# Kernel optimization log

Measured on AMD Instinct MI355X. Metric: run time of the kernel, lower is better.

## Reference

```python
import jax, jax.numpy as jnp
import numpy as np

N, E, HID, ED, L, H, D = 65536, 262144, 256, 64, 2, 8, 32
FF = 4 * HID
A_START = 8192  # first action gripper node; nodes [A_START:] are the T*K action nodes


def _ln(x, s, b, eps=1e-5):
    mu = jnp.mean(x, -1, keepdims=True)
    var = jnp.var(x, -1, keepdims=True)
    return (x - mu) * jax.lax.rsqrt(var + eps) * s + b


def _gnn_forward(x, edge_attr, edge_index, Wq, Wk, Wv, WeK, WeV, Wo,
                 ln1_s, ln1_b, ffn_w1, ffn_b1, ffn_w2, ffn_b2, ln2_s, ln2_b):
    # Hetero graph transformer over the single ('gripper','action','gripper') relation:
    # per-layer edge-indexed gather -> multi-head attention with edge features ->
    # segment softmax over incoming edges -> scatter-aggregate -> residual/LN/FFN.
    n = x.shape[0]
    e = edge_attr.shape[0]
    src, dst = edge_index[0], edge_index[1]
    inv_sqrt_d = np.float32(1.0 / np.sqrt(D))
    for l in range(Wq.shape[0]):
        q = (x @ Wq[l]).reshape(n, H, D)
        k = (x @ Wk[l]).reshape(n, H, D)
        v = (x @ Wv[l]).reshape(n, H, D)
        kj = k[src] + (edge_attr @ WeK[l]).reshape(e, H, D)  # [E,H,D] gathered keys + edge bias
        vj = v[src] + (edge_attr @ WeV[l]).reshape(e, H, D)
        score = jnp.einsum('ehd,ehd->eh', q[dst], kj) * inv_sqrt_d  # [E,H]
        smax = jax.ops.segment_max(score, dst, num_segments=n)
        p = jnp.exp(score - smax[dst])
        denom = jax.ops.segment_sum(p, dst, num_segments=n)
        alpha = p / denom[dst]  # segment softmax over incoming edges
        agg = jax.ops.segment_sum((alpha[..., None] * vj).reshape(e, H * D), dst, num_segments=n)
        x = _ln(x + agg @ Wo[l], ln1_s[l], ln1_b[l])
        hid = jax.nn.gelu(x @ ffn_w1[l] + ffn_b1[l], approximate=False) @ ffn_w2[l] + ffn_b2[l]
        x = _ln(x + hid, ln2_s[l], ln2_b[l])
    return x


def setup_inputs() -> dict:
    key = jax.random.key(0)
    ks = iter(jax.random.split(key, 16))
    w = lambda shape: jax.random.normal(next(ks), shape, jnp.float32) * 0.05
    return {
        "all_gripper_feats": jax.random.normal(next(ks), (N, HID), jnp.float32),
        "edge_attr": jax.random.normal(next(ks), (E, ED), jnp.float32),
        "Wq": w((L, HID, H * D)), "Wk": w((L, HID, H * D)), "Wv": w((L, HID, H * D)),
        "WeK": w((L, ED, H * D)), "WeV": w((L, ED, H * D)), "Wo": w((L, H * D, HID)),
        "ln1_s": jnp.ones((L, HID), jnp.float32), "ln1_b": jnp.zeros((L, HID), jnp.float32),
        "ffn_w1": w((L, HID, FF)), "ffn_b1": jnp.zeros((L, FF), jnp.float32),
        "ffn_w2": w((L, FF, HID)), "ffn_b2": jnp.zeros((L, HID), jnp.float32),
        "ln2_s": jnp.ones((L, HID), jnp.float32), "ln2_b": jnp.zeros((L, HID), jnp.float32),
        "head_w1": w((HID, HID)), "head_b1": jnp.zeros((HID,), jnp.float32),
        "head_w2": w((HID, 7)), "head_b2": jnp.zeros((7,), jnp.float32),
        "edge_index": jax.random.randint(next(ks), (2, E), 0, N),
        "action_start": A_START,
    }


def reference(all_gripper_feats, edge_attr, Wq, Wk, Wv, WeK, WeV, Wo,
              ln1_s, ln1_b, ffn_w1, ffn_b1, ffn_w2, ffn_b2, ln2_s, ln2_b,
              head_w1, head_b1, head_w2, head_b2, edge_index, action_start):
    x = _gnn_forward(all_gripper_feats, edge_attr, edge_index, Wq, Wk, Wv, WeK, WeV, Wo,
                     ln1_s, ln1_b, ffn_w1, ffn_b1, ffn_w2, ffn_b2, ln2_s, ln2_b)
    a = x[action_start:]  # action gripper nodes (T*K, hidden)
    return jax.nn.gelu(a @ head_w1 + head_b1, approximate=False) @ head_w2 + head_b2  # (T*K, 7)
```

## Files before the change

kernel.cpp:

```cpp
#include <hip/hip_runtime.h>
#include <hip/hip_bf16.h>
#include <math.h>

#define NN     65536
#define NE     262144
#define HIDN   256
#define EDIM   64
#define NHEAD  8
#define FFN    1024
#define ASTART 8192
#define NACT   (NN - ASTART)
#define NCH    32768
#define NCHP   (NCH + 128)
#define NCHUNK (NE / NCH)
#define DPC    (NN / NCHUNK)
#define RCH    32768

typedef __attribute__((ext_vector_type(8))) short short8;
typedef __attribute__((ext_vector_type(4))) short short4v;
typedef __attribute__((ext_vector_type(4))) float float4v;
typedef __hip_bfloat16 bf16;

__device__ __forceinline__ float b2f(short s) {
    union { unsigned u; float f; } c;
    c.u = ((unsigned)(unsigned short)s) << 16;
    return c.f;
}
__device__ __forceinline__ short f2b(float f) {
    __hip_bfloat16 h = __float2bfloat16(f);
    return *reinterpret_cast<short*>(&h);
}
__device__ __forceinline__ float gelu_fast(float v) {
    const float x  = v * 0.70710678118654752f;
    const float ax = fabsf(x);
    const float t  = __builtin_amdgcn_rcpf(1.0f + 0.3275911f * ax);
    const float y  = t * (0.254829592f + t * (-0.284496736f + t * (1.421413741f +
                     t * (-1.453152027f + t * 1.061405429f))));
    const float e  = __expf(-x * x);
    float erf = 1.0f - y * e;
    erf = copysignf(erf, x);
    return 0.5f * v * (1.0f + erf);
}
__device__ __forceinline__ void gload16(const void* g, void* l) {
    __builtin_amdgcn_global_load_lds(
        (const __attribute__((address_space(1))) void*)(uintptr_t)g,
        (__attribute__((address_space(3))) void*)(unsigned)(uintptr_t)l,
        16, 0, 0);
}

__global__ void convert_kernel(const float* __restrict__ src,
                               bf16* __restrict__ dst, int n) {
    int i = blockIdx.x * 256 + threadIdx.x;
    if (i < n) dst[i] = __float2bfloat16(src[i]);
}
__global__ void convert4_kernel(const float* __restrict__ src,
                                bf16* __restrict__ dst, int n4) {
    int i = blockIdx.x * 256 + threadIdx.x;
    if (i >= n4) return;
    float4v f = *(const float4v*)(src + (size_t)i * 4);
    short4v o;
    #pragma unroll
    for (int j = 0; j < 4; ++j) o[j] = f2b(f[j]);
    *(short4v*)((short*)dst + (size_t)i * 4) = o;
}

__global__ void transpose_kernel(const float* __restrict__ src,
                                 bf16* __restrict__ dst, int R, int Cc) {
    int idx = blockIdx.x * 256 + threadIdx.x;
    if (idx >= R * Cc) return;
    int r = idx / Cc, c = idx - r * Cc;
    dst[(size_t)c * R + r] = __float2bfloat16(src[idx]);
}

__global__ void hist_kernel(const int* __restrict__ dstI, int* __restrict__ cnt) {
    int i = blockIdx.x * 256 + threadIdx.x;
    if (i < NE) atomicAdd(&cnt[dstI[i]], 1);
}
__global__ void scan1_kernel(const int* __restrict__ cnt, int* __restrict__ rp,
                             int* __restrict__ bsum) {
    __shared__ int s[256];
    int t = threadIdx.x, i = blockIdx.x * 256 + t;
    int v = cnt[i]; s[t] = v; __syncthreads();
    for (int off = 1; off < 256; off <<= 1) {
        int x = (t >= off) ? s[t - off] : 0; __syncthreads();
        s[t] += x; __syncthreads();
    }
    rp[i] = s[t] - v;
    if (t == 255) bsum[blockIdx.x] = s[255];
}
__global__ void scan2_kernel(int* __restrict__ bsum) {
    __shared__ int s[256];
    int t = threadIdx.x; int v = bsum[t]; s[t] = v; __syncthreads();
    for (int off = 1; off < 256; off <<= 1) {
        int x = (t >= off) ? s[t - off] : 0; __syncthreads();
        s[t] += x; __syncthreads();
    }
    bsum[t] = s[t] - v;
}
__global__ void scan3_kernel(int* __restrict__ rp, const int* __restrict__ bsum,
                             int* __restrict__ cursor) {
    int i = blockIdx.x * 256 + threadIdx.x;
    int v = rp[i] + bsum[i >> 8];
    rp[i] = v; cursor[i] = v;
    if (i == 0) rp[NN] = NE;
}
__global__ void scatter_kernel(const int* __restrict__ srcI, const int* __restrict__ dstI,
                               int* __restrict__ cursor, int* __restrict__ perm,
                               int* __restrict__ src_s, int* __restrict__ dst_s) {
    int e = blockIdx.x * 256 + threadIdx.x;
    if (e >= NE) return;
    int d = dstI[e];
    int pos = atomicAdd(&cursor[d], 1);
    perm[pos] = e; src_s[pos] = srcI[e]; dst_s[pos] = d;
}

template<int AMODE, bool DO_GELU>
__global__ __launch_bounds__(256) void gemm_kernel(
    const void* __restrict__ A,
    const bf16* __restrict__ BT,
    const bf16* __restrict__ bias,
    bf16* __restrict__ C,
    int M, int Nn, int K,
    const int* __restrict__ perm, int permN)
{
    __shared__ __align__(16) short Ls[4][128 * 32];

    const int gx   = gridDim.x;
    const int nwg  = gx * gridDim.y;
    const int orig = blockIdx.y * gx + blockIdx.x;
    const int q8   = nwg >> 3, r8 = nwg & 7;
    const int xcd  = orig & 7, rk = orig >> 3;
    const int nid  = (xcd < r8 ? xcd * (q8 + 1) : r8 * (q8 + 1) + (xcd - r8) * q8) + rk;
    const int by   = nid / gx;
    const int bx   = nid - by * gx;

    const int t    = threadIdx.x;
    const int wave = t >> 6;
    const int lane = t & 63;
    const int l15  = lane & 15;
    const int quad = lane >> 4;
    const int wm   = (wave & 1) * 64;
    const int wn   = (wave >> 1) * 64;
    const int bm   = by * 128;
    const int bn   = bx * 128;
    const int srow = t >> 2;
    const int sw   = srow & 3;
    const int scolB = ((t & 3) ^ sw) * 8;
    const int scolA = (t & 3) * 8;

    const short* Ab = (const short*)A  + (size_t)(bm + srow) * K + scolB;
    const short* Bb = (const short*)BT + (size_t)(bn + srow) * K + scolB;
    const float* Af0 = nullptr;
    const float* Af1 = nullptr;
    if (AMODE == 1) {
        Af0 = (const float*)A + (size_t)(bm + srow) * K + scolA;
        Af1 = Af0 + (size_t)64 * K;
    } else if (AMODE == 2) {
        int i0 = bm + srow;       if (i0 >= permN) i0 = permN - 1;
        int i1 = bm + 64 + srow;  if (i1 >= permN) i1 = permN - 1;
        const int pr0 = perm[i0];
        const int pr1 = perm[i1];
        Af0 = (const float*)A + (size_t)pr0 * K + scolA;
        Af1 = (const float*)A + (size_t)pr1 * K + scolA;
    }
    const int offW  = wave * 1024;
    const int offTs = (t * 16) ^ (sw << 4);
    const int qs16  = (quad ^ (l15 & 3)) * 16;

    float4v acc[4][4];
    #pragma unroll
    for (int i = 0; i < 4; ++i)
        #pragma unroll
        for (int j = 0; j < 4; ++j) acc[i][j] = (float4v){0.f, 0.f, 0.f, 0.f};

    const int nt = K >> 5;

    auto STAGE = [&](int b, int k0) {
        char* lA = (char*)Ls[b];
        char* lB = (char*)Ls[2 + b];
        if (AMODE == 0) {
            gload16(Ab + k0,                  lA + offW);
            gload16(Ab + (size_t)64 * K + k0, lA + 4096 + offW);
        } else {
            #pragma unroll
            for (int i = 0; i < 2; ++i) {
                const float* s = (i ? Af1 : Af0) + k0;
                float4v f0 = *(const float4v*)s;
                float4v f1 = *(const float4v*)(s + 4);
                short8 w;
                #pragma unroll
                for (int j = 0; j < 4; ++j) { w[j] = f2b(f0[j]); w[4 + j] = f2b(f1[j]); }
                *(short8*)(lA + i * 4096 + offTs) = w;
            }
        }
        gload16(Bb + k0,                  lB + offW);
        gload16(Bb + (size_t)64 * K + k0, lB + 4096 + offW);
    };

    STAGE(0, 0);
    __syncthreads();

    for (int kt = 0; kt < nt; ++kt) {
        const int cur = kt & 1;
        if (kt + 1 < nt) STAGE(cur ^ 1, (kt + 1) * 32);

        const char* lA = (const char*)Ls[cur];
        const char* lB = (const char*)Ls[2 + cur];
        short8 afr[4], bfr[4];
        #pragma unroll
        for (int i = 0; i < 4; ++i)
            afr[i] = *(const short8*)(lA + (wm + i * 16 + l15) * 64 + qs16);
        #pragma unroll
        for (int j = 0; j < 4; ++j)
            bfr[j] = *(const short8*)(lB + (wn + j * 16 + l15) * 64 + qs16);
        #pragma unroll
        for (int i = 0; i < 4; ++i)
            #pragma unroll
            for (int j = 0; j < 4; ++j)
                acc[i][j] = __builtin_amdgcn_mfma_f32_16x16x32_bf16(afr[i], bfr[j], acc[i][j], 0, 0, 0);
        __syncthreads();
    }

    short* Ct = (short*)Ls;
    #pragma unroll
    for (int j = 0; j < 4; ++j) {
        const int col  = wn + j * 16 + l15;
        const int pc   = col ^ (quad << 4);
        const float bv = bias ? b2f(((const short*)bias)[bn + col]) : 0.0f;
        #pragma unroll
        for (int i = 0; i < 4; ++i) {
            const int row0 = wm + i * 16 + quad * 4;
            #pragma unroll
            for (int r = 0; r < 4; ++r) {
                float v = acc[i][j][r] + bv;
                if (DO_GELU) v = gelu_fast(v);
                Ct[(row0 + r) * 128 + pc] = f2b(v);
            }
        }
    }
    __syncthreads();
    #pragma unroll
    for (int it = 0; it < 8; ++it) {
        const int row = wave * 32 + it + ((lane >> 4) << 3);
        const int cs  = (lane & 15) * 8;
        const int pcs = cs ^ (((row >> 2) & 3) << 4);
        short8 w = *(const short8*)&Ct[row * 128 + pcs];
        *(short8*)((short*)C + (size_t)(bm + row) * Nn + bn + cs) = w;
    }
}

__global__ __launch_bounds__(256) void score_kernel(
    const bf16* __restrict__ q, const bf16* __restrict__ k,
    const bf16* __restrict__ eK,
    const int* __restrict__ src_s, const int* __restrict__ dst_s,
    short* __restrict__ pbuf, int e0, int qkstride)
{
    const int p = e0 + blockIdx.x * 4 + (threadIdx.x >> 6);
    const int lane = threadIdx.x & 63;
    const int s = src_s[p], d = dst_s[p];
    const int off = lane * 4;

    const short4v qv = *(const short4v*)((const short*)q  + (size_t)d * qkstride + off);
    const short4v kv = *(const short4v*)((const short*)k  + (size_t)s * qkstride + off);
    const short4v ev = *(const short4v*)((const short*)eK + (size_t)(p - e0) * HIDN + off);
    float x = 0.f;
    #pragma unroll
    for (int j = 0; j < 4; ++j) x += b2f(qv[j]) * (b2f(kv[j]) + b2f(ev[j]));
    x += __shfl_xor(x, 1);
    x += __shfl_xor(x, 2);
    x += __shfl_xor(x, 4);
    if ((lane & 7) == 0) {
        const float sc = fminf(fmaxf(x * 0.17677669529663689f, -30.f), 30.f);
        pbuf[(size_t)p * NHEAD + (lane >> 3)] = f2b(expf(sc));
    }
}

__global__ __launch_bounds__(256) void agg_kernel(
    const short* __restrict__ pbuf, const bf16* __restrict__ v,
    const bf16* __restrict__ eV,
    const int* __restrict__ src_s, const int* __restrict__ rp,
    float* __restrict__ agg, int e0, int e1x, int dlo)
{
    const int d = dlo + blockIdx.x * 4 + (threadIdx.x >> 6);
    const int lane = threadIdx.x & 63;
    const int es = rp[d], ee = rp[d + 1];
    if (es < e0 || es >= e1x) return;
    const int h = lane >> 3, off = lane * 4;

    float a0 = 0.f, a1 = 0.f, a2 = 0.f, a3 = 0.f;
    if (es < ee) {
        float den = 0.f;
        for (int p = es; p < ee; ++p) den += b2f(pbuf[(size_t)p * NHEAD + h]);
        const float rden = 1.0f / den;
        for (int p = es; p < ee; ++p) {
            const float al = b2f(pbuf[(size_t)p * NHEAD + h]) * rden;
            const int s = src_s[p];
            const short4v vv = *(const short4v*)((const short*)v  + (size_t)s * HIDN + off);
            const short4v ev = *(const short4v*)((const short*)eV + (size_t)(p - e0) * HIDN + off);
            a0 += al * (b2f(vv[0]) + b2f(ev[0]));
            a1 += al * (b2f(vv[1]) + b2f(ev[1]));
            a2 += al * (b2f(vv[2]) + b2f(ev[2]));
            a3 += al * (b2f(vv[3]) + b2f(ev[3]));
        }
    }
    *(float4v*)(agg + (size_t)d * HIDN + off) = (float4v){a0, a1, a2, a3};
}

__global__ __launch_bounds__(256) void ln_kernel(
    bf16* __restrict__ x, const bf16* __restrict__ t,
    const bf16* __restrict__ sc, const bf16* __restrict__ bi, int r0)
{
    const int row = r0 + blockIdx.x * 4 + (threadIdx.x >> 6);
    const int lane = threadIdx.x & 63;
    const size_t base = (size_t)row * HIDN + lane * 4;
    const size_t tbase = (size_t)(row - r0) * HIDN + lane * 4;
    const short4v xv = *(const short4v*)((const short*)x + base);
    const short4v tv = *(const short4v*)((const short*)t + tbase);
    float v[4];
    #pragma unroll
    for (int j = 0; j < 4; ++j) v[j] = b2f(xv[j]) + b2f(tv[j]);
    float sum = v[0] + v[1] + v[2] + v[3];
    float ssq = v[0]*v[0] + v[1]*v[1] + v[2]*v[2] + v[3]*v[3];
    #pragma unroll
    for (int m = 1; m < 64; m <<= 1) { sum += __shfl_xor(sum, m); ssq += __shfl_xor(ssq, m); }
    const float mean = sum * (1.0f / 256.0f);
    const float var  = fmaxf(ssq * (1.0f / 256.0f) - mean * mean, 0.0f);
    const float rstd = rsqrtf(var + 1e-5f);
    const short4v sv = *(const short4v*)((const short*)sc + lane * 4);
    const short4v bv = *(const short4v*)((const short*)bi + lane * 4);
    short4v out;
    #pragma unroll
    for (int j = 0; j < 4; ++j)
        out[j] = f2b((v[j] - mean) * rstd * b2f(sv[j]) + b2f(bv[j]));
    *(short4v*)((short*)x + base) = out;
}

__global__ __launch_bounds__(256) void head2_kernel(
    const bf16* __restrict__ h1, const bf16* __restrict__ w2T,
    const bf16* __restrict__ b2, float* __restrict__ out)
{
    const int row = blockIdx.x * 4 + (threadIdx.x >> 6);
    const int lane = threadIdx.x & 63;
    const int off = lane * 4;
    const short4v hv = *(const short4v*)((const short*)h1 + (size_t)row * HIDN + off);
    float hf[4];
    #pragma unroll
    for (int j = 0; j < 4; ++j) hf[j] = b2f(hv[j]);
    float acc[7];
    #pragma unroll
    for (int jc = 0; jc < 7; ++jc) {
        const short4v wv = *(const short4v*)((const short*)w2T + jc * HIDN + off);
        float a = hf[0]*b2f(wv[0]) + hf[1]*b2f(wv[1]) + hf[2]*b2f(wv[2]) + hf[3]*b2f(wv[3]);
        #pragma unroll
        for (int m = 1; m < 64; m <<= 1) a += __shfl_xor(a, m);
        acc[jc] = a;
    }
    if (lane < 7) {
        float r = lane == 0 ? acc[0] : lane == 1 ? acc[1] : lane == 2 ? acc[2] :
                  lane == 3 ? acc[3] : lane == 4 ? acc[4] : lane == 5 ? acc[5] : acc[6];
        out[(size_t)row * 7 + lane] = r + b2f(((const short*)b2)[lane]);
    }
}

extern "C" void kernel_launch(void* const* d_in, const int* in_sizes, int n_in,
                              void* d_out, int out_size, void* d_ws, size_t ws_size,
                              hipStream_t stream)
{
    const float* xin   = (const float*)d_in[0];
    const float* eattr = (const float*)d_in[1];
    const float* Wq    = (const float*)d_in[2];
    const float* Wk    = (const float*)d_in[3];
    const float* Wv    = (const float*)d_in[4];
    const float* WeK   = (const float*)d_in[5];
    const float* WeV   = (const float*)d_in[6];
    const float* Wo    = (const float*)d_in[7];
    const float* ln1s  = (const float*)d_in[8];
    const float* ln1b  = (const float*)d_in[9];
    const float* fw1   = (const float*)d_in[10];
    const float* fb1   = (const float*)d_in[11];
    const float* fw2   = (const float*)d_in[12];
    const float* fb2   = (const float*)d_in[13];
    const float* ln2s  = (const float*)d_in[14];
    const float* ln2b  = (const float*)d_in[15];
    const float* hw1   = (const float*)d_in[16];
    const float* hb1   = (const float*)d_in[17];
    const float* hw2   = (const float*)d_in[18];
    const float* hb2   = (const float*)d_in[19];
    const int*  eidx   = (const int*)d_in[20];
    const int*  srcI   = eidx;
    const int*  dstI   = eidx + NE;

    char* base = (char*)d_ws;
    size_t off = 0;
    auto carve = [&](size_t bytes) -> char* {
        char* p = base + off;
        off += (bytes + 255) & ~(size_t)255;
        return p;
    };
    bf16*  x_b    = (bf16*) carve((size_t)NN * HIDN * 2);
    bf16*  qk_b   = (bf16*) carve((size_t)NN * 2 * HIDN * 2);
    bf16*  v_b    = (bf16*) carve((size_t)NN * HIDN * 2);
    bf16*  echunk = (bf16*) carve((size_t)NCHP * HIDN * 2);
    short* pbuf   = (short*)carve((size_t)NE * NHEAD * 2);
    int*   perm   = (int*)  carve((size_t)NE * 4);
    int*   src_s  = (int*)  carve((size_t)NE * 4);
    int*   dst_s  = (int*)  carve((size_t)NE * 4);
    int*   rowp   = (int*)  carve((size_t)(NN + 1) * 4);
    bf16*  WqkT   = (bf16*) carve((size_t)2 * HIDN * HIDN * 2);
    bf16*  WvT    = (bf16*) carve((size_t)HIDN * HIDN * 2);
    bf16*  WoT    = (bf16*) carve((size_t)HIDN * HIDN * 2);
    bf16*  WeKT   = (bf16*) carve((size_t)HIDN * EDIM * 2);
    bf16*  WeVT   = (bf16*) carve((size_t)HIDN * EDIM * 2);
    bf16*  W1T    = (bf16*) carve((size_t)FFN * HIDN * 2);
    bf16*  W2T    = (bf16*) carve((size_t)HIDN * FFN * 2);
    bf16*  HW1T   = (bf16*) carve((size_t)HIDN * HIDN * 2);
    bf16*  HW2T   = (bf16*) carve((size_t)8 * HIDN * 2);
    bf16*  c_ln1s = (bf16*) carve((size_t)2 * HIDN * 2);
    bf16*  c_ln1b = (bf16*) carve((size_t)2 * HIDN * 2);
    bf16*  c_ln2s = (bf16*) carve((size_t)2 * HIDN * 2);
    bf16*  c_ln2b = (bf16*) carve((size_t)2 * HIDN * 2);
    bf16*  c_fb1  = (bf16*) carve((size_t)2 * FFN * 2);
    bf16*  c_fb2  = (bf16*) carve((size_t)2 * HIDN * 2);
    bf16*  c_hb1  = (bf16*) carve((size_t)HIDN * 2);
    bf16*  c_hb2  = (bf16*) carve((size_t)16 * 2);
    if (off > ws_size) return;

    int* cnt    = (int*)echunk;
    int* cursor = cnt + NN;
    int* bsum   = cursor + NN;
    float* agg    = (float*)qk_b;
    bf16*  tmp_b  = v_b;
    bf16*  hid    = qk_b;
    bf16*  ffnout = v_b;

    const int TB = 256;
    #define GRID1(n) dim3(((n) + TB - 1) / TB)

    convert4_kernel<<<GRID1(NN * HIDN / 4), TB, 0, stream>>>(xin, x_b, NN * HIDN / 4);
    convert_kernel<<<GRID1(2 * HIDN), TB, 0, stream>>>(ln1s, c_ln1s, 2 * HIDN);
    convert_kernel<<<GRID1(2 * HIDN), TB, 0, stream>>>(ln1b, c_ln1b, 2 * HIDN);
    convert_kernel<<<GRID1(2 * HIDN), TB, 0, stream>>>(ln2s, c_ln2s, 2 * HIDN);
    convert_kernel<<<GRID1(2 * HIDN), TB, 0, stream>>>(ln2b, c_ln2b, 2 * HIDN);
    convert_kernel<<<GRID1(2 * FFN), TB, 0, stream>>>(fb1, c_fb1, 2 * FFN);
    convert_kernel<<<GRID1(2 * HIDN), TB, 0, stream>>>(fb2, c_fb2, 2 * HIDN);
    convert_kernel<<<GRID1(HIDN), TB, 0, stream>>>(hb1, c_hb1, HIDN);
    convert_kernel<<<1, TB, 0, stream>>>(hb2, c_hb2, 7);
    transpose_kernel<<<GRID1(HIDN * HIDN), TB, 0, stream>>>(hw1, HW1T, HIDN, HIDN);
    transpose_kernel<<<GRID1(HIDN * 7), TB, 0, stream>>>(hw2, HW2T, HIDN, 7);

    hipMemsetAsync(cnt, 0, (size_t)NN * 4, stream);
    hist_kernel<<<GRID1(NE), TB, 0, stream>>>(dstI, cnt);
    scan1_kernel<<<NN / 256, 256, 0, stream>>>(cnt, rowp, bsum);
    scan2_kernel<<<1, 256, 0, stream>>>(bsum);
    scan3_kernel<<<NN / 256, 256, 0, stream>>>(rowp, bsum, cursor);
    scatter_kernel<<<GRID1(NE), TB, 0, stream>>>(srcI, dstI, cursor, perm, src_s, dst_s);

    for (int l = 0; l < 2; ++l) {
        transpose_kernel<<<GRID1(HIDN * HIDN), TB, 0, stream>>>(Wq + (size_t)l*HIDN*HIDN, WqkT, HIDN, HIDN);
        transpose_kernel<<<GRID1(HIDN * HIDN), TB, 0, stream>>>(Wk + (size_t)l*HIDN*HIDN, WqkT + (size_t)HIDN*HIDN, HIDN, HIDN);
        transpose_kernel<<<GRID1(HIDN * HIDN), TB, 0, stream>>>(Wv + (size_t)l*HIDN*HIDN, WvT, HIDN, HIDN);
        transpose_kernel<<<GRID1(EDIM * HIDN), TB, 0, stream>>>(WeK + (size_t)l*EDIM*HIDN, WeKT, EDIM, HIDN);
        transpose_kernel<<<GRID1(EDIM * HIDN), TB, 0, stream>>>(WeV + (size_t)l*EDIM*HIDN, WeVT, EDIM, HIDN);
        transpose_kernel<<<GRID1(HIDN * HIDN), TB, 0, stream>>>(Wo + (size_t)l*HIDN*HIDN, WoT, HIDN, HIDN);
        transpose_kernel<<<GRID1(HIDN * FFN),  TB, 0, stream>>>(fw1 + (size_t)l*HIDN*FFN, W1T, HIDN, FFN);
        transpose_kernel<<<GRID1(FFN * HIDN),  TB, 0, stream>>>(fw2 + (size_t)l*FFN*HIDN, W2T, FFN, HIDN);

        gemm_kernel<0, false><<<dim3((2*HIDN)/128, NN/128), TB, 0, stream>>>(x_b, WqkT, nullptr, qk_b, NN, 2*HIDN, HIDN, nullptr, 0);
        gemm_kernel<0, false><<<dim3(HIDN/128, NN/128), TB, 0, stream>>>(x_b, WvT, nullptr, v_b, NN, HIDN, HIDN, nullptr, 0);

        for (int c = 0; c < NCHUNK; ++c) {
            gemm_kernel<2, false><<<dim3(HIDN/128, NCH/128), TB, 0, stream>>>(
                eattr, WeKT, nullptr, echunk, NCH, HIDN, EDIM, perm + (size_t)c * NCH, NE - c * NCH);
            score_kernel<<<NCH / 4, TB, 0, stream>>>(qk_b, qk_b + HIDN, echunk, src_s, dst_s, pbuf, c * NCH, 2 * HIDN);
        }

        for (int c = 0; c < NCHUNK; ++c) {
            gemm_kernel<2, false><<<dim3(HIDN/128, NCHP/128), TB, 0, stream>>>(
                eattr, WeVT, nullptr, echunk, NCHP, HIDN, EDIM, perm + (size_t)c * NCH, NE - c * NCH);
            const int dlo = (c == 0) ? 0 : (c - 1) * DPC;
            const int dhi = (c == NCHUNK - 1) ? NN : (c + 2) * DPC;
            const int e1x = (c == NCHUNK - 1) ? NE + 1 : (c + 1) * NCH;
            agg_kernel<<<(dhi - dlo) / 4, TB, 0, stream>>>(
                pbuf, v_b, echunk, src_s, rowp, agg, c * NCH, e1x, dlo);
        }

        gemm_kernel<1, false><<<dim3(HIDN/128, NN/128), TB, 0, stream>>>(agg, WoT, nullptr, tmp_b, NN, HIDN, HIDN, nullptr, 0);
        ln_kernel<<<NN / 4, TB, 0, stream>>>(x_b, tmp_b, c_ln1s + (size_t)l * HIDN, c_ln1b + (size_t)l * HIDN, 0);

        for (int r0 = 0; r0 < NN; r0 += RCH) {
            gemm_kernel<0, true ><<<dim3(FFN/128, RCH/128), TB, 0, stream>>>(
                x_b + (size_t)r0 * HIDN, W1T, c_fb1 + (size_t)l * FFN, hid, RCH, FFN, HIDN, nullptr, 0);
            gemm_kernel<0, false><<<dim3(HIDN/128, RCH/128), TB, 0, stream>>>(
                hid, W2T, c_fb2 + (size_t)l * HIDN, ffnout, RCH, HIDN, FFN, nullptr, 0);
            ln_kernel<<<RCH / 4, TB, 0, stream>>>(x_b, ffnout, c_ln2s + (size_t)l * HIDN, c_ln2b + (size_t)l * HIDN, r0);
        }
    }

    gemm_kernel<0, true><<<dim3(HIDN/128, NACT/128), TB, 0, stream>>>(
        x_b + (size_t)ASTART * HIDN, HW1T, c_hb1, hid, NACT, HIDN, HIDN, nullptr, 0);
    head2_kernel<<<NACT / 4, TB, 0, stream>>>(hid, HW2T, c_hb2, (float*)d_out);
}
```

Baseline: 1.505 ms.

## Deepen GEMM global-to-LDS pipeline to four-stage ring with vmcnt waits

For the direct bf16 A path, the GEMM now uses a 4-slot LDS ring with three tiles in flight. It waits with explicit vmcnt counts and one barrier per k-step, replacing the double buffer that needed a full sync each iteration. The aim is to hide global-load latency behind MFMA work. This doubles LDS use, which may lower occupancy, and correctness depends on the hand-tuned waitcnt values and on the ring ordering being free of races.

```diff
diff --git a/kernel.cpp b/kernel.cpp
--- a/kernel.cpp
+++ b/kernel.cpp
@@ -123,7 +123,8 @@
     int M, int Nn, int K,
     const int* __restrict__ perm, int permN)
 {
-    __shared__ __align__(16) short Ls[4][128 * 32];
+    constexpr int RING = (AMODE == 0) ? 4 : 2;
+    __shared__ __align__(16) short Ls[2 * RING][128 * 32];
 
     const int gx   = gridDim.x;
     const int nwg  = gx * gridDim.y;
@@ -177,7 +178,7 @@
 
     auto STAGE = [&](int b, int k0) {
         char* lA = (char*)Ls[b];
-        char* lB = (char*)Ls[2 + b];
+        char* lB = (char*)Ls[RING + b];
         if (AMODE == 0) {
             gload16(Ab + k0,                  lA + offW);
             gload16(Ab + (size_t)64 * K + k0, lA + 4096 + offW);
@@ -197,15 +198,9 @@
         gload16(Bb + (size_t)64 * K + k0, lB + 4096 + offW);
     };
 
-    STAGE(0, 0);
-    __syncthreads();
-
-    for (int kt = 0; kt < nt; ++kt) {
-        const int cur = kt & 1;
-        if (kt + 1 < nt) STAGE(cur ^ 1, (kt + 1) * 32);
-
-        const char* lA = (const char*)Ls[cur];
-        const char* lB = (const char*)Ls[2 + cur];
+    auto COMPUTE = [&](int b) {
+        const char* lA = (const char*)Ls[b];
+        const char* lB = (const char*)Ls[RING + b];
         short8 afr[4], bfr[4];
         #pragma unroll
         for (int i = 0; i < 4; ++i)
@@ -218,7 +213,40 @@
             #pragma unroll
             for (int j = 0; j < 4; ++j)
                 acc[i][j] = __builtin_amdgcn_mfma_f32_16x16x32_bf16(afr[i], bfr[j], acc[i][j], 0, 0, 0);
+    };
+
+    if (AMODE == 0) {
+        STAGE(0, 0);
+        if (nt > 1) STAGE(1, 32);
+        if (nt > 2) STAGE(2, 64);
+        for (int kt = 0; kt < nt - 2; ++kt) {
+            asm volatile("s_waitcnt vmcnt(8) lgkmcnt(0)" ::: "memory");
+            __builtin_amdgcn_sched_barrier(0);
+            __builtin_amdgcn_s_barrier();
+            __builtin_amdgcn_sched_barrier(0);
+            STAGE((kt + 3) & 3, (kt + 3) * 32);
+            COMPUTE(kt & 3);
+        }
+        asm volatile("s_waitcnt vmcnt(4) lgkmcnt(0)" ::: "memory");
+        __builtin_amdgcn_sched_barrier(0);
+        __builtin_amdgcn_s_barrier();
+        __builtin_amdgcn_sched_barrier(0);
+        COMPUTE((nt - 2) & 3);
+        asm volatile("s_waitcnt vmcnt(0) lgkmcnt(0)" ::: "memory");
+        __builtin_amdgcn_sched_barrier(0);
+        __builtin_amdgcn_s_barrier();
+        __builtin_amdgcn_sched_barrier(0);
+        COMPUTE((nt - 1) & 3);
         __syncthreads();
+    } else {
+        STAGE(0, 0);
+        __syncthreads();
+        for (int kt = 0; kt < nt; ++kt) {
+            const int cur = kt & 1;
+            if (kt + 1 < nt) STAGE(cur ^ 1, (kt + 1) * 32);
+            COMPUTE(cur);
+            __syncthreads();
+        }
     }
 
     short* Ct = (short*)Ls;
```

Result: no change. 1.523 ms (+1.2%).
